# Optimization experiments

Hardware: AMD Instinct MI355X
Metric: run time of the kernel (lower is better)

Reference implementation:

```python
import jax, jax.numpy as jnp
import numpy as np

EPS = 1e-5

def _g(x):
    # continuous candidate activation used by log-space minGRU (g(x)=x+0.5 if x>=0 else sigmoid(x))
    return jnp.where(x >= 0, x + 0.5, jax.nn.sigmoid(x))

def _layernorm(x, gamma, beta):
    mu = jnp.mean(x, axis=-1, keepdims=True)
    var = jnp.var(x, axis=-1, keepdims=True)
    return (x - mu) * jax.lax.rsqrt(var + EPS) * gamma + beta

def _min_gru(x, w, b):
    # x: (B,T,D) -> (B,T,D); linear recurrence h_t = (1-z_t)*h_{t-1} + z_t*g(htilde_t), h_0 = 0
    hg = x @ w + b                       # (B,T,2D)
    hidden, gate = jnp.split(hg, 2, axis=-1)
    z = jax.nn.sigmoid(gate)
    a = 1.0 - z
    bb = z * _g(hidden)
    def combine(c1, c2):
        a1, b1 = c1
        a2, b2 = c2
        return (a1 * a2, a2 * b1 + b2)
    _, h = jax.lax.associative_scan(combine, (a, bb), axis=1)
    return h

def _gru_block(x, w, b, g, bta):
    return _layernorm(_min_gru(x, w, b), g, bta)

def setup_inputs() -> dict:
    key = jax.random.key(0)
    ks = jax.random.split(key, 16)
    B, T, X, H, D, M = 8, 8192, 64, 128, 5, 10
    s_in = 1.0 / np.sqrt(X)
    s_h = 1.0 / np.sqrt(H)
    inp = {
        "x": jax.random.normal(ks[0], (B, T, X), jnp.float32),
        "embed_w": jax.random.uniform(ks[1], (X, H), jnp.float32, -s_in, s_in),
        "embed_b": jax.random.uniform(ks[2], (H,), jnp.float32, -s_in, s_in),
        "ln0_g": jnp.ones((H,), jnp.float32),
        "ln0_b": jnp.zeros((H,), jnp.float32),
        "proj_w": jax.random.uniform(ks[3], (H, D * M), jnp.float32, -s_h, s_h),
        "proj_b": jax.random.uniform(ks[4], (D * M,), jnp.float32, -s_h, s_h),
    }
    for i in (1, 2, 3):
        inp[f"gru{i}_w"] = jax.random.uniform(ks[4 + 2 * i], (H, 2 * H), jnp.float32, -s_h, s_h)
        inp[f"gru{i}_b"] = jax.random.uniform(ks[5 + 2 * i], (2 * H,), jnp.float32, -s_h, s_h)
        inp[f"ln{i}_g"] = jnp.ones((H,), jnp.float32)
        inp[f"ln{i}_b"] = jnp.zeros((H,), jnp.float32)
    return inp

def reference(x, embed_w, embed_b, ln0_g, ln0_b,
              gru1_w, gru1_b, ln1_g, ln1_b,
              gru2_w, gru2_b, ln2_g, ln2_b,
              gru3_w, gru3_b, ln3_g, ln3_b,
              proj_w, proj_b):
    D_CH, M_CH = 5, 10
    h = jax.nn.leaky_relu(x @ embed_w + embed_b, 0.01)
    h = _layernorm(h, ln0_g, ln0_b)
    h = _gru_block(h, gru1_w, gru1_b, ln1_g, ln1_b)
    h = _gru_block(h, gru2_w, gru2_b, ln2_g, ln2_b)
    h = _gru_block(h, gru3_w, gru3_b, ln3_g, ln3_b)
    out = h @ proj_w + proj_b                      # (B,T,D_CH*M_CH)
    B, T, _ = out.shape
    return jax.nn.softplus(out.reshape(B, T, D_CH, M_CH))
```

## Files before the change

kernel.cpp:

```cpp
#include <hip/hip_runtime.h>
#include <math.h>

#define BB 8
#define TT 8192
#define XX 64
#define HH 128
#define CHUNK 32
#define NC (TT/CHUNK)

typedef __attribute__((ext_vector_type(8))) short short8;
typedef __attribute__((ext_vector_type(4))) float f32x4;

__device__ __forceinline__ float sigm(float x){
  return __builtin_amdgcn_rcpf(1.0f + __expf(-x));
}
__device__ __forceinline__ unsigned short f2bf(float f){
  unsigned u = __float_as_uint(f);
  return (unsigned short)((u + 0x7fffu + ((u>>16)&1u)) >> 16);
}
__device__ __forceinline__ float bf2f(unsigned b){ return __uint_as_float(b << 16); }

__global__ __launch_bounds__(256) void prep_kernel(
    const float* __restrict__ w1, const float* __restrict__ w2, const float* __restrict__ w3,
    const float* __restrict__ ew, const float* __restrict__ pw,
    unsigned short* __restrict__ wt, unsigned short* __restrict__ wt_e, unsigned short* __restrict__ wt_p)
{
  int idx = blockIdx.x*256 + threadIdx.x;
  if (idx < 98304) {
    int l = idx >> 15;
    int e = idx & 32767;
    int k = e >> 8;
    int col = e & 255;
    const float* w = (l==0) ? w1 : ((l==1) ? w2 : w3);
    float v = w[e];
    unsigned byte = ((unsigned)col*128u + (unsigned)k)*2u;
    byte ^= (unsigned)((col & 7) << 4);
    wt[(size_t)l*32768 + (byte >> 1)] = f2bf(v);
  } else if (idx < 106496) {
    int e = idx - 98304;
    int col = e >> 6, k = e & 63;
    float v = ew[k*HH + col];
    unsigned byte = ((unsigned)e*2u) ^ (unsigned)((col & 7) << 4);
    wt_e[byte >> 1] = f2bf(v);
  } else if (idx < 114688) {
    int e = idx - 106496;
    int col = e >> 7, k = e & 127;
    float v = (col < 50) ? pw[k*50 + col] : 0.f;
    unsigned byte = ((unsigned)e*2u) ^ (unsigned)((col & 7) << 4);
    wt_p[byte >> 1] = f2bf(v);
  }
}

__global__ __launch_bounds__(256) void embed_mfma_kernel(
    const float* __restrict__ x, const unsigned short* __restrict__ wt_e,
    const float* __restrict__ eb, const float* __restrict__ g, const float* __restrict__ be,
    unsigned short* __restrict__ hout)
{
  __shared__ short8 wlds[1024];
  int tid = threadIdx.x;
  const short8* wsrc = (const short8*)wt_e;
  #pragma unroll
  for (int i = 0; i < 4; ++i) wlds[i*256 + tid] = wsrc[i*256 + tid];

  int wid = tid >> 6, lane = tid & 63;
  int lr = lane & 15, lg = lane >> 4;
  int sx = (lane & 7) << 4;
  long row0 = (long)(blockIdx.x*4 + wid)*32;

  short8 af[2][2];
  #pragma unroll
  for (int m = 0; m < 2; ++m)
    #pragma unroll
    for (int s = 0; s < 2; ++s) {
      const float* xp = x + (row0 + m*16 + lr)*XX + s*32 + lg*8;
      float4 u0 = *(const float4*)xp;
      float4 u1 = *(const float4*)(xp + 4);
      short8 t;
      t[0]=f2bf(u0.x); t[1]=f2bf(u0.y); t[2]=f2bf(u0.z); t[3]=f2bf(u0.w);
      t[4]=f2bf(u1.x); t[5]=f2bf(u1.y); t[6]=f2bf(u1.z); t[7]=f2bf(u1.w);
      af[m][s] = t;
    }
  __syncthreads();

  const char* wbase = (const char*)wlds;
  f32x4 acc[2][8];
  #pragma unroll
  for (int m = 0; m < 2; ++m)
    #pragma unroll
    for (int np = 0; np < 8; ++np) acc[m][np] = (f32x4){0.f,0.f,0.f,0.f};

  #pragma unroll
  for (int np = 0; np < 8; ++np) {
    int col = np*16 + lr;
    #pragma unroll
    for (int s = 0; s < 2; ++s) {
      short8 bh = *(const short8*)(wbase + ((col*128 + s*64 + lg*16) ^ sx));
      #pragma unroll
      for (int m = 0; m < 2; ++m)
        acc[m][np] = __builtin_amdgcn_mfma_f32_16x16x32_bf16(af[m][s], bh, acc[m][np], 0, 0, 0);
    }
  }

  float gamv[8], betv[8], biasv[8];
  #pragma unroll
  for (int np = 0; np < 8; ++np) {
    int col = np*16 + lr;
    gamv[np] = g[col]; betv[np] = be[col]; biasv[np] = eb[col];
  }

  #pragma unroll
  for (int m = 0; m < 2; ++m) {
    float s4[4], q4[4];
    #pragma unroll
    for (int r = 0; r < 4; ++r) { s4[r] = 0.f; q4[r] = 0.f; }
    #pragma unroll
    for (int np = 0; np < 8; ++np)
      #pragma unroll
      for (int r = 0; r < 4; ++r) {
        float v = acc[m][np][r] + biasv[np];
        v = v > 0.f ? v : 0.01f*v;
        acc[m][np][r] = v;
        s4[r] += v; q4[r] += v*v;
      }
    #pragma unroll
    for (int off = 1; off < 16; off <<= 1)
      #pragma unroll
      for (int r = 0; r < 4; ++r) {
        s4[r] += __shfl_xor(s4[r], off);
        q4[r] += __shfl_xor(q4[r], off);
      }
    #pragma unroll
    for (int r = 0; r < 4; ++r) {
      float mu = s4[r] * (1.f/128.f);
      float var = q4[r] * (1.f/128.f) - mu*mu;
      float rs = rsqrtf(var + 1e-5f);
      long row = row0 + m*16 + lg*4 + r;
      #pragma unroll
      for (int np = 0; np < 8; ++np)
        hout[row*HH + np*16 + lr] = f2bf((acc[m][np][r]-mu)*rs*gamv[np] + betv[np]);
    }
  }
}

__global__ __launch_bounds__(256) void gru_mm_kernel(
    const unsigned short* __restrict__ h, const unsigned short* __restrict__ wt,
    const float* __restrict__ bias,
    unsigned* __restrict__ ab, float* __restrict__ AsT, float* __restrict__ BsT)
{
  __shared__ short8 wlds[4096];
  int tid = threadIdx.x;
  int wid = tid >> 6, lane = tid & 63;
  int chunk = blockIdx.x*4 + wid;
  int b = chunk >> 8, c = chunk & 255;
  long row0 = (long)b*TT + (long)c*CHUNK;
  int lr = lane & 15, lg = lane >> 4;
  int sx = (lane & 7) << 4;

  short8 af[2][4];
  #pragma unroll
  for (int m = 0; m < 2; ++m)
    #pragma unroll
    for (int s = 0; s < 4; ++s)
      af[m][s] = *(const short8*)(h + (row0 + m*16 + lr)*HH + s*32 + lg*8);

  const short8* wsrc = (const short8*)wt;
  #pragma unroll
  for (int i = 0; i < 16; ++i) wlds[i*256 + tid] = wsrc[i*256 + tid];
  __syncthreads();

  const char* wbase = (const char*)wlds;
  #pragma unroll 2
  for (int np = 0; np < 8; ++np) {
    f32x4 acch[2], accg[2];
    #pragma unroll
    for (int m = 0; m < 2; ++m) { acch[m] = (f32x4){0.f,0.f,0.f,0.f}; accg[m] = (f32x4){0.f,0.f,0.f,0.f}; }
    int rh = np*16 + lr;
    int rg = rh + 128;
    #pragma unroll
    for (int s = 0; s < 4; ++s) {
      short8 bh = *(const short8*)(wbase + ((rh*256 + s*64 + lg*16) ^ sx));
      short8 bg = *(const short8*)(wbase + ((rg*256 + s*64 + lg*16) ^ sx));
      #pragma unroll
      for (int m = 0; m < 2; ++m) {
        acch[m] = __builtin_amdgcn_mfma_f32_16x16x32_bf16(af[m][s], bh, acch[m], 0, 0, 0);
        accg[m] = __builtin_amdgcn_mfma_f32_16x16x32_bf16(af[m][s], bg, accg[m], 0, 0, 0);
      }
    }
    int col = np*16 + lr;
    float bh0 = bias[col], bg0 = bias[HH + col];
    float At[2], Bt[2];
    #pragma unroll
    for (int m = 0; m < 2; ++m) {
      float A4 = 1.f, B4 = 0.f;
      #pragma unroll
      for (int r = 0; r < 4; ++r) {
        float hid = acch[m][r] + bh0;
        float z = sigm(accg[m][r] + bg0);
        float gv = hid >= 0.f ? hid + 0.5f : sigm(hid);
        float av = 1.f - z, bv = z*gv;
        size_t grow = (size_t)(row0 + m*16 + lg*4 + r);
        ab[grow*HH + col] = (unsigned)f2bf(av) | ((unsigned)f2bf(bv) << 16);
        A4 *= av; B4 = av*B4 + bv;
      }
      #pragma unroll
      for (int off = 1; off < 4; off <<= 1) {
        float pa = __shfl_up(A4, off*16);
        float pb = __shfl_up(B4, off*16);
        float na = pa*A4, nb = A4*pb + B4;
        if (lg >= off) { A4 = na; B4 = nb; }
      }
      At[m] = __shfl(A4, 48 + lr);
      Bt[m] = __shfl(B4, 48 + lr);
    }
    if (lane < 16) {
      float Ac = At[0]*At[1];
      float Bc = At[1]*Bt[0] + Bt[1];
      size_t sidx = ((size_t)b*128 + col)*256 + c;
      AsT[sidx] = Ac;
      BsT[sidx] = Bc;
    }
  }
}

__global__ __launch_bounds__(256) void scan2_kernel(
    const float* __restrict__ AsT, const float* __restrict__ BsT, float* __restrict__ carT)
{
  int wid = threadIdx.x >> 6, lane = threadIdx.x & 63;
  int s = blockIdx.x*4 + wid;
  float4 Av = ((const float4*)(AsT + (size_t)s*256))[lane];
  float4 Bv = ((const float4*)(BsT + (size_t)s*256))[lane];
  float Ai = Av.x, Bi = Bv.x;
  Bi = Av.y*Bi + Bv.y; Ai = Av.y*Ai;
  Bi = Av.z*Bi + Bv.z; Ai = Av.z*Ai;
  Bi = Av.w*Bi + Bv.w; Ai = Av.w*Ai;
  #pragma unroll
  for (int off = 1; off < 64; off <<= 1) {
    float pA = __shfl_up(Ai, off);
    float pB = __shfl_up(Bi, off);
    if (lane >= off) { Bi = Ai*pB + Bi; Ai = Ai*pA; }
  }
  float exB = __shfl_up(Bi, 1);
  if (lane == 0) exB = 0.f;
  float run = exB;
  float4 cv;
  cv.x = run; run = Av.x*run + Bv.x;
  cv.y = run; run = Av.y*run + Bv.y;
  cv.z = run; run = Av.z*run + Bv.z;
  cv.w = run;
  ((float4*)(carT + (size_t)s*256))[lane] = cv;
}

__global__ __launch_bounds__(256) void apply_kernel(
    const unsigned* __restrict__ ab, const float* __restrict__ carT,
    const float* __restrict__ g, const float* __restrict__ be,
    unsigned short* __restrict__ hout)
{
  int tid = threadIdx.x, wid = tid >> 6, lane = tid & 63;
  int chunk = blockIdx.x*4 + wid;
  int b = chunk >> 8, c = chunk & 255;
  float2 hc;
  hc.x = carT[((size_t)b*128 + 2*lane    )*256 + c];
  hc.y = carT[((size_t)b*128 + 2*lane + 1)*256 + c];
  float2 gam = ((const float2*)g)[lane];
  float2 bet = ((const float2*)be)[lane];
  size_t rowbase = (size_t)chunk*CHUNK;
  for (int gq = 0; gq < 4; ++gq) {
    uint2 v[8];
    #pragma unroll
    for (int j = 0; j < 8; ++j)
      v[j] = ((const uint2*)(ab + (rowbase + gq*8 + j)*HH))[lane];
    #pragma unroll
    for (int j = 0; j < 8; ++j) {
      float ax = bf2f(v[j].x & 0xffffu), bx = bf2f(v[j].x >> 16);
      float ay = bf2f(v[j].y & 0xffffu), by = bf2f(v[j].y >> 16);
      hc.x = ax*hc.x + bx;
      hc.y = ay*hc.y + by;
      float s = hc.x + hc.y, q = hc.x*hc.x + hc.y*hc.y;
      #pragma unroll
      for (int m = 1; m < 64; m <<= 1) { s += __shfl_xor(s, m); q += __shfl_xor(q, m); }
      float mu = s * (1.f/128.f);
      float var = q * (1.f/128.f) - mu*mu;
      float rs = rsqrtf(var + 1e-5f);
      unsigned o = (unsigned)f2bf((hc.x-mu)*rs*gam.x + bet.x)
                 | ((unsigned)f2bf((hc.y-mu)*rs*gam.y + bet.y) << 16);
      ((unsigned*)hout)[(rowbase + gq*8 + j)*64 + lane] = o;
    }
  }
}

__global__ __launch_bounds__(256) void apply_proj_kernel(
    const unsigned* __restrict__ ab, const float* __restrict__ carT,
    const float* __restrict__ g, const float* __restrict__ be,
    const unsigned short* __restrict__ wt_p, const float* __restrict__ pb,
    float* __restrict__ out)
{
  __shared__ short8 wlds[1024];
  __shared__ unsigned hlds[4*2048];
  int tid = threadIdx.x, wid = tid >> 6, lane = tid & 63;
  const short8* wsrc = (const short8*)wt_p;
  #pragma unroll
  for (int i = 0; i < 4; ++i) wlds[i*256 + tid] = wsrc[i*256 + tid];

  int chunk = blockIdx.x*4 + wid;
  int b = chunk >> 8, c = chunk & 255;
  float2 hc;
  hc.x = carT[((size_t)b*128 + 2*lane    )*256 + c];
  hc.y = carT[((size_t)b*128 + 2*lane + 1)*256 + c];
  float2 gam = ((const float2*)g)[lane];
  float2 bet = ((const float2*)be)[lane];
  size_t rowbase = (size_t)chunk*CHUNK;
  unsigned* myh = hlds + wid*2048;

  for (int gq = 0; gq < 4; ++gq) {
    uint2 v[8];
    #pragma unroll
    for (int j = 0; j < 8; ++j)
      v[j] = ((const uint2*)(ab + (rowbase + gq*8 + j)*HH))[lane];
    #pragma unroll
    for (int j = 0; j < 8; ++j) {
      float ax = bf2f(v[j].x & 0xffffu), bx = bf2f(v[j].x >> 16);
      float ay = bf2f(v[j].y & 0xffffu), by = bf2f(v[j].y >> 16);
      hc.x = ax*hc.x + bx;
      hc.y = ay*hc.y + by;
      float s = hc.x + hc.y, q = hc.x*hc.x + hc.y*hc.y;
      #pragma unroll
      for (int m2 = 1; m2 < 64; m2 <<= 1) { s += __shfl_xor(s, m2); q += __shfl_xor(q, m2); }
      float mu = s * (1.f/128.f);
      float var = q * (1.f/128.f) - mu*mu;
      float rs = rsqrtf(var + 1e-5f);
      unsigned o = (unsigned)f2bf((hc.x-mu)*rs*gam.x + bet.x)
                 | ((unsigned)f2bf((hc.y-mu)*rs*gam.y + bet.y) << 16);
      int t = gq*8 + j;
      myh[(t*64 + lane) ^ ((t & 7) << 2)] = o;
    }
  }
  __syncthreads();

  int lr = lane & 15, lg = lane >> 4;
  int sx = (lane & 7) << 4;
  short8 af[2][4];
  #pragma unroll
  for (int m = 0; m < 2; ++m)
    #pragma unroll
    for (int s = 0; s < 4; ++s) {
      int row = m*16 + lr;
      af[m][s] = *(const short8*)(myh + (((row*64) + s*16 + lg*4) ^ ((row & 7) << 2)));
    }

  const char* wbase = (const char*)wlds;
  f32x4 acc[2][4];
  #pragma unroll
  for (int m = 0; m < 2; ++m)
    #pragma unroll
    for (int np = 0; np < 4; ++np) acc[m][np] = (f32x4){0.f,0.f,0.f,0.f};

  #pragma unroll
  for (int np = 0; np < 4; ++np) {
    int col = np*16 + lr;
    #pragma unroll
    for (int s = 0; s < 4; ++s) {
      short8 bh = *(const short8*)(wbase + ((col*256 + s*64 + lg*16) ^ sx));
      #pragma unroll
      for (int m = 0; m < 2; ++m)
        acc[m][np] = __builtin_amdgcn_mfma_f32_16x16x32_bf16(af[m][s], bh, acc[m][np], 0, 0, 0);
    }
  }

  #pragma unroll
  for (int np = 0; np < 4; ++np) {
    int col = np*16 + lr;
    bool act = col < 50;
    float bias = act ? pb[col] : 0.f;
    #pragma unroll
    for (int m = 0; m < 2; ++m)
      #pragma unroll
      for (int r = 0; r < 4; ++r) {
        float v = acc[m][np][r] + bias;
        float sp = fmaxf(v, 0.f) + log1pf(__expf(-fabsf(v)));
        if (act) out[(rowbase + m*16 + lg*4 + r)*50 + col] = sp;
      }
  }
}

extern "C" void kernel_launch(void* const* d_in, const int* in_sizes, int n_in,
                              void* d_out, int out_size, void* d_ws, size_t ws_size,
                              hipStream_t stream) {
  const float* x    = (const float*)d_in[0];
  const float* ew   = (const float*)d_in[1];
  const float* eb   = (const float*)d_in[2];
  const float* ln0g = (const float*)d_in[3];
  const float* ln0b = (const float*)d_in[4];
  const float* pw   = (const float*)d_in[5];
  const float* pb   = (const float*)d_in[6];
  float* out = (float*)d_out;

  size_t nBT  = (size_t)BB*TT*HH;
  size_t nSum = (size_t)BB*NC*HH;
  unsigned short* h  = (unsigned short*)d_ws;
  unsigned*       ab = (unsigned*)(h + nBT);
  float* AsT  = (float*)(ab + nBT);
  float* BsT  = AsT + nSum;
  float* carT = BsT + nSum;
  unsigned short* wt   = (unsigned short*)(carT + nSum);
  unsigned short* wt_e = wt + 3*32768;
  unsigned short* wt_p = wt_e + 8192;

  prep_kernel<<<448, 256, 0, stream>>>((const float*)d_in[7], (const float*)d_in[11],
                                       (const float*)d_in[15], ew, pw, wt, wt_e, wt_p);
  embed_mfma_kernel<<<(BB*TT)/128, 256, 0, stream>>>(x, wt_e, eb, ln0g, ln0b, h);

  for (int l = 0; l < 3; ++l) {
    const float* gb = (const float*)d_in[8 + 4*l];
    const float* lg = (const float*)d_in[9 + 4*l];
    const float* lb = (const float*)d_in[10 + 4*l];
    gru_mm_kernel<<<(BB*NC)/4, 256, 0, stream>>>(h, wt + (size_t)l*32768, gb, ab, AsT, BsT);
    scan2_kernel<<<256, 256, 0, stream>>>(AsT, BsT, carT);
    if (l < 2) {
      apply_kernel<<<(BB*NC)/4, 256, 0, stream>>>(ab, carT, lg, lb, h);
    } else {
      apply_proj_kernel<<<(BB*NC)/4, 256, 0, stream>>>(ab, carT, lg, lb, wt_p, pb, out);
    }
  }
}
```

Baseline: 141.9 us.

## Fuse GRU apply/layernorm with next layer's matmul, keeping activations in LDS

The separate apply kernel and next-layer gru_mm kernel become one apply_mm_kernel for the middle layers. It recomputes the hidden states, layernorms them into a swizzled LDS tile, then runs the next layer's MFMA gate matmul directly from LDS, writing new ab values and chunk summaries. This removes the global round-trip of the bf16 activation tensor and two kernel launches. In exchange it uses more LDS per block (weights plus activations), which may limit occupancy, and it overwrites ab in place.

```diff
diff --git a/kernel.cpp b/kernel.cpp
--- a/kernel.cpp
+++ b/kernel.cpp
@@ -250,12 +250,20 @@
   ((float4*)(carT + (size_t)s*256))[lane] = cv;
 }
 
-__global__ __launch_bounds__(256) void apply_kernel(
-    const unsigned* __restrict__ ab, const float* __restrict__ carT,
+__global__ __launch_bounds__(256) void apply_mm_kernel(
+    unsigned* __restrict__ ab, const float* __restrict__ carT,
     const float* __restrict__ g, const float* __restrict__ be,
-    unsigned short* __restrict__ hout)
+    const unsigned short* __restrict__ wt, const float* __restrict__ bias,
+    float* __restrict__ AsT, float* __restrict__ BsT)
 {
+  __shared__ short8 wlds[4096];
+  __shared__ unsigned hlds[4*2048];
   int tid = threadIdx.x, wid = tid >> 6, lane = tid & 63;
+
+  const short8* wsrc = (const short8*)wt;
+  #pragma unroll
+  for (int i = 0; i < 16; ++i) wlds[i*256 + tid] = wsrc[i*256 + tid];
+
   int chunk = blockIdx.x*4 + wid;
   int b = chunk >> 8, c = chunk & 255;
   float2 hc;
@@ -264,6 +272,8 @@
   float2 gam = ((const float2*)g)[lane];
   float2 bet = ((const float2*)be)[lane];
   size_t rowbase = (size_t)chunk*CHUNK;
+  unsigned* myh = hlds + wid*2048;
+
   for (int gq = 0; gq < 4; ++gq) {
     uint2 v[8];
     #pragma unroll
@@ -277,13 +287,80 @@
       hc.y = ay*hc.y + by;
       float s = hc.x + hc.y, q = hc.x*hc.x + hc.y*hc.y;
       #pragma unroll
-      for (int m = 1; m < 64; m <<= 1) { s += __shfl_xor(s, m); q += __shfl_xor(q, m); }
+      for (int m2 = 1; m2 < 64; m2 <<= 1) { s += __shfl_xor(s, m2); q += __shfl_xor(q, m2); }
       float mu = s * (1.f/128.f);
       float var = q * (1.f/128.f) - mu*mu;
       float rs = rsqrtf(var + 1e-5f);
       unsigned o = (unsigned)f2bf((hc.x-mu)*rs*gam.x + bet.x)
                  | ((unsigned)f2bf((hc.y-mu)*rs*gam.y + bet.y) << 16);
-      ((unsigned*)hout)[(rowbase + gq*8 + j)*64 + lane] = o;
+      int t = gq*8 + j;
+      myh[(t*64 + lane) ^ ((t & 7) << 2)] = o;
+    }
+  }
+  __syncthreads();
+
+  long row0 = (long)b*TT + (long)c*CHUNK;
+  int lr = lane & 15, lg = lane >> 4;
+  int sx = (lane & 7) << 4;
+  short8 af[2][4];
+  #pragma unroll
+  for (int m = 0; m < 2; ++m)
+    #pragma unroll
+    for (int s = 0; s < 4; ++s) {
+      int row = m*16 + lr;
+      af[m][s] = *(const short8*)(myh + (((row*64) + s*16 + lg*4) ^ ((row & 7) << 2)));
+    }
+
+  const char* wbase = (const char*)wlds;
+  #pragma unroll 2
+  for (int np = 0; np < 8; ++np) {
+    f32x4 acch[2], accg[2];
+    #pragma unroll
+    for (int m = 0; m < 2; ++m) { acch[m] = (f32x4){0.f,0.f,0.f,0.f}; accg[m] = (f32x4){0.f,0.f,0.f,0.f}; }
+    int rh = np*16 + lr;
+    int rg = rh + 128;
+    #pragma unroll
+    for (int s = 0; s < 4; ++s) {
+      short8 bh = *(const short8*)(wbase + ((rh*256 + s*64 + lg*16) ^ sx));
+      short8 bg = *(const short8*)(wbase + ((rg*256 + s*64 + lg*16) ^ sx));
+      #pragma unroll
+      for (int m = 0; m < 2; ++m) {
+        acch[m] = __builtin_amdgcn_mfma_f32_16x16x32_bf16(af[m][s], bh, acch[m], 0, 0, 0);
+        accg[m] = __builtin_amdgcn_mfma_f32_16x16x32_bf16(af[m][s], bg, accg[m], 0, 0, 0);
+      }
+    }
+    int col = np*16 + lr;
+    float bh0 = bias[col], bg0 = bias[HH + col];
+    float At[2], Bt[2];
+    #pragma unroll
+    for (int m = 0; m < 2; ++m) {
+      float A4 = 1.f, B4 = 0.f;
+      #pragma unroll
+      for (int r = 0; r < 4; ++r) {
+        float hid = acch[m][r] + bh0;
+        float z = sigm(accg[m][r] + bg0);
+        float gv = hid >= 0.f ? hid + 0.5f : sigm(hid);
+        float av = 1.f - z, bv = z*gv;
+        size_t grow = (size_t)(row0 + m*16 + lg*4 + r);
+        ab[grow*HH + col] = (unsigned)f2bf(av) | ((unsigned)f2bf(bv) << 16);
+        A4 *= av; B4 = av*B4 + bv;
+      }
+      #pragma unroll
+      for (int off = 1; off < 4; off <<= 1) {
+        float pa = __shfl_up(A4, off*16);
+        float pb = __shfl_up(B4, off*16);
+        float na = pa*A4, nb = A4*pb + B4;
+        if (lg >= off) { A4 = na; B4 = nb; }
+      }
+      At[m] = __shfl(A4, 48 + lr);
+      Bt[m] = __shfl(B4, 48 + lr);
+    }
+    if (lane < 16) {
+      float Ac = At[0]*At[1];
+      float Bc = At[1]*Bt[0] + Bt[1];
+      size_t sidx = ((size_t)b*128 + col)*256 + c;
+      AsT[sidx] = Ac;
+      BsT[sidx] = Bc;
     }
   }
 }
@@ -409,16 +486,19 @@
                                        (const float*)d_in[15], ew, pw, wt, wt_e, wt_p);
   embed_mfma_kernel<<<(BB*TT)/128, 256, 0, stream>>>(x, wt_e, eb, ln0g, ln0b, h);
 
-  for (int l = 0; l < 3; ++l) {
-    const float* gb = (const float*)d_in[8 + 4*l];
-    const float* lg = (const float*)d_in[9 + 4*l];
-    const float* lb = (const float*)d_in[10 + 4*l];
-    gru_mm_kernel<<<(BB*NC)/4, 256, 0, stream>>>(h, wt + (size_t)l*32768, gb, ab, AsT, BsT);
-    scan2_kernel<<<256, 256, 0, stream>>>(AsT, BsT, carT);
-    if (l < 2) {
-      apply_kernel<<<(BB*NC)/4, 256, 0, stream>>>(ab, carT, lg, lb, h);
-    } else {
-      apply_proj_kernel<<<(BB*NC)/4, 256, 0, stream>>>(ab, carT, lg, lb, wt_p, pb, out);
-    }
-  }
-}
+  gru_mm_kernel<<<(BB*NC)/4, 256, 0, stream>>>(h, wt, (const float*)d_in[8], ab, AsT, BsT);
+  scan2_kernel<<<256, 256, 0, stream>>>(AsT, BsT, carT);
+
+  apply_mm_kernel<<<(BB*NC)/4, 256, 0, stream>>>(ab, carT,
+      (const float*)d_in[9], (const float*)d_in[10],
+      wt + 32768, (const float*)d_in[12], AsT, BsT);
+  scan2_kernel<<<256, 256, 0, stream>>>(AsT, BsT, carT);
+
+  apply_mm_kernel<<<(BB*NC)/4, 256, 0, stream>>>(ab, carT,
+      (const float*)d_in[13], (const float*)d_in[14],
+      wt + 65536, (const float*)d_in[16], AsT, BsT);
+  scan2_kernel<<<256, 256, 0, stream>>>(AsT, BsT, carT);
+
+  apply_proj_kernel<<<(BB*NC)/4, 256, 0, stream>>>(ab, carT,
+      (const float*)d_in[17], (const float*)d_in[18], wt_p, pb, out);
+}
```

Measured after the change: 152.7 us. +7.6%, slower.
